# Performance work log

Measured on AMD Instinct MI355X. Metric: run time of the kernel, lower is better.

Reference implementation:

```python
import jax, jax.numpy as jnp
import numpy as np

OUT = 7          # roi_align output size
SR = 2           # sampling_ratio
SCALE = 1.0 / 16.0
T_OUT = 16       # F.interpolate temporal target
EPS = 1e-6


def setup_inputs() -> dict:
    key = jax.random.key(0)
    ks = jax.random.split(key, 12)
    B, Cin, Cout, T, H, W = 1, 1536, 3072, 16, 14, 14
    y = jax.random.normal(ks[0], (B, Cin, T, H, W), jnp.float32)
    x_t = jax.random.normal(ks[1], (B, Cout, T, H, W), jnp.float32)
    # ROIs in 224x224 image coords (spatial_scale = 1/16): one [1,4] box per frame
    x1 = jax.random.uniform(ks[2], (T,), minval=0.0, maxval=112.0)
    y1 = jax.random.uniform(ks[3], (T,), minval=0.0, maxval=112.0)
    x2 = jnp.minimum(x1 + jax.random.uniform(ks[4], (T,), minval=80.0, maxval=112.0), 224.0)
    y2 = jnp.minimum(y1 + jax.random.uniform(ks[5], (T,), minval=80.0, maxval=112.0), 224.0)
    rois = jnp.stack([x1, y1, x2, y2], axis=-1)[:, None, :]  # [T,1,4]
    conv_w = jax.random.normal(ks[6], (Cout, Cin), jnp.float32) * 0.02
    conv_b = jax.random.normal(ks[7], (Cout,), jnp.float32) * 0.02
    gamma = 1.0 + 0.1 * jax.random.normal(ks[8], (Cout,), jnp.float32)
    beta = 0.1 * jax.random.normal(ks[9], (Cout,), jnp.float32)
    run_mean = 0.1 * jax.random.normal(ks[10], (Cout,), jnp.float32)
    run_var = jax.random.uniform(ks[11], (Cout,), minval=0.5, maxval=1.5)
    return dict(y=y, x_t=x_t, rois=rois, conv_w=conv_w, conv_b=conv_b,
                gamma=gamma, beta=beta, run_mean=run_mean, run_var=run_var)


def _bilinear_sample(img, ys, xs):
    # img: [C,H,W]; ys: [Sy]; xs: [Sx] -> [C,Sy,Sx]; torchvision roi_align semantics
    C, H, W = img.shape
    oy = (ys < -1.0) | (ys > H)
    ox = (xs < -1.0) | (xs > W)
    yc = jnp.clip(ys, 0.0, H - 1)
    xc = jnp.clip(xs, 0.0, W - 1)
    y0 = jnp.floor(yc).astype(jnp.int32)
    x0 = jnp.floor(xc).astype(jnp.int32)
    y1i = jnp.minimum(y0 + 1, H - 1)
    x1i = jnp.minimum(x0 + 1, W - 1)
    ly = yc - y0
    lx = xc - x0
    g = lambda yi, xi: img[:, yi[:, None], xi[None, :]]  # [C,Sy,Sx]
    wy0, wy1 = (1.0 - ly)[:, None], ly[:, None]
    wx0, wx1 = (1.0 - lx)[None, :], lx[None, :]
    val = (wy0 * wx0 * g(y0, x0) + wy0 * wx1 * g(y0, x1i)
           + wy1 * wx0 * g(y1i, x0) + wy1 * wx1 * g(y1i, x1i))
    mask = (~oy)[:, None] & (~ox)[None, :]
    return jnp.where(mask[None], val, 0.0)


def _roi_align(feat, boxes):
    # feat: [N,C,H,W]; boxes: [N,4] (one box per image, aligned=False, sampling_ratio=2)
    N, C, H, W = feat.shape
    b = boxes * SCALE
    bx1, by1, bx2, by2 = b[:, 0], b[:, 1], b[:, 2], b[:, 3]
    rw = jnp.maximum(bx2 - bx1, 1.0)
    rh = jnp.maximum(by2 - by1, 1.0)
    bw, bh = rw / OUT, rh / OUT
    # sample positions per bin: (bin + (i+0.5)/SR) * bin_size
    pos = (jnp.arange(OUT, dtype=jnp.float32)[:, None]
           + (jnp.arange(SR, dtype=jnp.float32)[None, :] + 0.5) / SR).reshape(-1)  # [OUT*SR]
    ys = by1[:, None] + pos[None, :] * bh[:, None]
    xs = bx1[:, None] + pos[None, :] * bw[:, None]
    vals = jax.vmap(_bilinear_sample)(feat, ys, xs)  # [N,C,OUT*SR,OUT*SR]
    return vals.reshape(N, C, OUT, SR, OUT, SR).mean(axis=(3, 5))


def reference(y, x_t, rois, conv_w, conv_b, gamma, beta, run_mean, run_var):
    B, Cout, T, Hf, Wf = x_t.shape
    # 1x1x1 Conv3d, stride (1,2,2)
    ys = y[:, :, :, ::2, ::2]                                   # [B,Cin,T,7,7]
    yp = jnp.einsum('bcthw,oc->bothw', ys, conv_w) + conv_b[None, :, None, None, None]
    # BatchNorm3d (eval, eps=1e-6) + GELU (exact)
    inv = gamma / jnp.sqrt(run_var + EPS)
    yp = (yp - run_mean[None, :, None, None, None]) * inv[None, :, None, None, None] \
         + beta[None, :, None, None, None]
    yp = jax.nn.gelu(yp, approximate=False)
    # nearest temporal interpolation to T_OUT (identity when Tin == 16)
    Tin = yp.shape[2]
    tidx = (jnp.arange(T_OUT) * Tin) // T_OUT
    yp = yp[:, :, tidx]                                          # [B,Cout,16,7,7]
    # fusion branch: roi_align over (B*T) frames
    ff = jnp.transpose(x_t, (0, 2, 1, 3, 4)).reshape(B * T, Cout, Hf, Wf)
    boxes = rois[:, 0, :]                                        # [T,4]
    mr = _roi_align(ff, boxes)                                   # [B*T,Cout,7,7]
    mr = jnp.transpose(mr.reshape(B, T, Cout, OUT, OUT), (0, 2, 1, 3, 4))
    weighted = yp * mr                                           # [B,Cout,16,7,7]
    # per-frame 7x7 scatter-write into zeros, same window logic as the torch loop
    bs = boxes * SCALE
    sxi = jnp.floor(bs[:, 0]).astype(jnp.int32)
    syi = jnp.floor(bs[:, 1]).astype(jnp.int32)
    exi = jnp.ceil(bs[:, 2]).astype(jnp.int32)
    eyi = jnp.ceil(bs[:, 3]).astype(jnp.int32)
    ml = jnp.where(sxi + 7 < 14, sxi, exi - 7)
    mt = jnp.where(syi + 7 < 14, syi, eyi - 7)
    def place(w_t, t_off, l_off):  # w_t: [B,Cout,7,7]
        z = jnp.zeros((B, Cout, Hf, Wf), w_t.dtype)
        return jax.lax.dynamic_update_slice(z, w_t, (0, 0, t_off, l_off))
    new_face = jax.vmap(place, in_axes=(2, 0, 0), out_axes=2)(weighted, mt, ml)
    return new_face + x_t
```

## Files before the change

### kernel.cpp

```cpp
#include <hip/hip_runtime.h>

#define KD 1536
#define ND 3072
#define MD 784
#define MPAD 832
#define TT 16

#define NB_ROI 768
#define NB_PACKA 384
#define NB_ZERO 1
#define NB_PACKB 1152
#define PREP_BLOCKS (NB_ROI + NB_PACKA + NB_ZERO + NB_PACKB)

typedef __attribute__((ext_vector_type(8))) short short8;
typedef __attribute__((ext_vector_type(4))) float floatx4;

__device__ __forceinline__ unsigned short f2bf(float f) {
    unsigned int x = __float_as_uint(f);
    unsigned int r = (x + 0x7fffu + ((x >> 16) & 1u)) >> 16;
    return (unsigned short)r;
}

__global__ __launch_bounds__(256) void prep_k(const float* __restrict__ y,
                                              const float* __restrict__ x_t,
                                              const float* __restrict__ rois,
                                              const float* __restrict__ conv_w,
                                              unsigned short* __restrict__ Ap,
                                              unsigned short* __restrict__ Bp,
                                              float* __restrict__ mr) {
    __shared__ float sm[64 * 197];
    __shared__ float wx0s[14], wx1s[14], wy0s[14], wy1s[14];
    __shared__ int x0s[14], x1s[14], y0s[14], y1s[14], vxs[14], vys[14];
    const int bid = blockIdx.x;
    const int tid = threadIdx.x;

    if (bid >= NB_ROI + NB_PACKA + NB_ZERO) {
        int pb = bid - (NB_ROI + NB_PACKA + NB_ZERO);
#pragma unroll
        for (int v = 0; v < 4; ++v) {
            size_t e = (size_t)pb * 4096 + v * 1024 + tid * 4;
            float4 w4 = *(const float4*)(conv_w + e);
            ushort4 o;
            o.x = f2bf(w4.x); o.y = f2bf(w4.y); o.z = f2bf(w4.z); o.w = f2bf(w4.w);
            *(ushort4*)(Bp + e) = o;
        }
        return;
    }
    if (bid == NB_ROI + NB_PACKA) {
        uint4 z = {0u, 0u, 0u, 0u};
        uint4* dst = (uint4*)(Ap + (size_t)MD * KD);
        for (int v = tid; v < (MPAD - MD) * KD / 8; v += 256) dst[v] = z;
        return;
    }
    if (bid >= NB_ROI) {
        int p = bid - NB_ROI;
        int t = p / 24, kc = p % 24;
        for (int f = tid; f < 64 * 196; f += 256) {
            int c = f / 196, pix = f % 196;
            sm[c * 197 + pix] = y[(size_t)(kc * 64 + c) * 3136 + t * 196 + pix];
        }
        __syncthreads();
        for (int item = tid; item < 64 * 49; item += 256) {
            int c = item & 63, ij = item >> 6;
            int i = ij / 7, j = ij % 7;
            Ap[(size_t)(t * 49 + ij) * KD + kc * 64 + c] =
                f2bf(sm[c * 197 + (2 * i) * 14 + 2 * j]);
        }
        return;
    }

    const int t = bid / 48;
    const int o0 = (bid % 48) * 64;

    if (tid < 14) {
        float b0 = rois[t * 4 + 0] * 0.0625f, b1 = rois[t * 4 + 1] * 0.0625f;
        float b2 = rois[t * 4 + 2] * 0.0625f, b3 = rois[t * 4 + 3] * 0.0625f;
        float rw = fmaxf(b2 - b0, 1.0f), rh = fmaxf(b3 - b1, 1.0f);
        float bw = rw * (1.0f / 7.0f), bh = rh * (1.0f / 7.0f);
        int p = tid;
        float pos = (float)(p >> 1) + 0.25f + 0.5f * (float)(p & 1);
        float xs = b0 + pos * bw;
        float ysv = b1 + pos * bh;
        vxs[p] = (xs >= -1.0f && xs <= 14.0f);
        vys[p] = (ysv >= -1.0f && ysv <= 14.0f);
        float xc = fminf(fmaxf(xs, 0.0f), 13.0f);
        float yc = fminf(fmaxf(ysv, 0.0f), 13.0f);
        int x0 = (int)floorf(xc), y0 = (int)floorf(yc);
        x0s[p] = x0; y0s[p] = y0;
        x1s[p] = min(x0 + 1, 13); y1s[p] = min(y0 + 1, 13);
        float lx = xc - (float)x0, ly = yc - (float)y0;
        wx0s[p] = 1.0f - lx; wx1s[p] = lx; wy0s[p] = 1.0f - ly; wy1s[p] = ly;
    }
    for (int f = tid; f < 64 * 196; f += 256) {
        int c = f / 196, pix = f % 196;
        sm[c * 197 + pix] = x_t[(size_t)(o0 + c) * 3136 + t * 196 + pix];
    }
    __syncthreads();
    for (int item = tid; item < 64 * 49; item += 256) {
        int c = item & 63, ij = item >> 6;
        int i = ij / 7, j = ij % 7;
        const float* base = &sm[c * 197];
        float sum = 0.0f;
#pragma unroll
        for (int s = 0; s < 2; ++s) {
            int p = 2 * i + s;
#pragma unroll
            for (int u = 0; u < 2; ++u) {
                int q = 2 * j + u;
                if (vys[p] && vxs[q]) {
                    float v00 = base[y0s[p] * 14 + x0s[q]];
                    float v01 = base[y0s[p] * 14 + x1s[q]];
                    float v10 = base[y1s[p] * 14 + x0s[q]];
                    float v11 = base[y1s[p] * 14 + x1s[q]];
                    sum += wy0s[p] * (wx0s[q] * v00 + wx1s[q] * v01) +
                           wy1s[p] * (wx0s[q] * v10 + wx1s[q] * v11);
                }
            }
        }
        mr[(size_t)(t * 49 + ij) * ND + o0 + c] = 0.25f * sum;
    }
}

__global__ __launch_bounds__(256) void gemm_k(const unsigned short* __restrict__ Ap,
                                              const unsigned short* __restrict__ Bp,
                                              const float* __restrict__ cb,
                                              const float* __restrict__ gm,
                                              const float* __restrict__ bt,
                                              const float* __restrict__ rm,
                                              const float* __restrict__ rv,
                                              float* __restrict__ mrW) {
    __shared__ unsigned short As[2][64][72];
    __shared__ unsigned short Bs[2][64][72];
    const int tid = threadIdx.x;
    const int n0 = blockIdx.x * 64;
    const int m0 = blockIdx.y * 64;
    const int wave = tid >> 6;
    const int lane = tid & 63;
    const int wm = wave >> 1, wn = wave & 1;
    const int l15 = lane & 15, quad = lane >> 4;

    floatx4 acc00 = {0.f, 0.f, 0.f, 0.f}, acc01 = {0.f, 0.f, 0.f, 0.f};
    floatx4 acc10 = {0.f, 0.f, 0.f, 0.f}, acc11 = {0.f, 0.f, 0.f, 0.f};

    const int srow = tid >> 3;
    const int sko = (tid & 7) * 8;
    const float4* agp0 = (const float4*)(Ap + (size_t)(m0 + srow) * KD + sko);
    const float4* agp1 = (const float4*)(Ap + (size_t)(m0 + srow + 32) * KD + sko);
    const float4* bgp0 = (const float4*)(Bp + (size_t)(n0 + srow) * KD + sko);
    const float4* bgp1 = (const float4*)(Bp + (size_t)(n0 + srow + 32) * KD + sko);

    float4 av0 = agp0[0], av1 = agp1[0], bv0 = bgp0[0], bv1 = bgp1[0];

    int p = 0;
    for (int kt = 0; kt < KD; kt += 64, p ^= 1) {
        *(float4*)(&As[p][srow][sko]) = av0;
        *(float4*)(&As[p][srow + 32][sko]) = av1;
        *(float4*)(&Bs[p][srow][sko]) = bv0;
        *(float4*)(&Bs[p][srow + 32][sko]) = bv1;
        __syncthreads();
        if (kt + 64 < KD) {
            int q = (kt >> 3) + 8;
            av0 = agp0[q]; av1 = agp1[q]; bv0 = bgp0[q]; bv1 = bgp1[q];
        }
#pragma unroll
        for (int ko = 0; ko < 2; ++ko) {
            short8 a0 = *(const short8*)(&As[p][wm * 32 + l15][ko * 32 + quad * 8]);
            short8 a1 = *(const short8*)(&As[p][wm * 32 + 16 + l15][ko * 32 + quad * 8]);
            short8 b0 = *(const short8*)(&Bs[p][wn * 32 + l15][ko * 32 + quad * 8]);
            short8 b1 = *(const short8*)(&Bs[p][wn * 32 + 16 + l15][ko * 32 + quad * 8]);
            acc00 = __builtin_amdgcn_mfma_f32_16x16x32_bf16(a0, b0, acc00, 0, 0, 0);
            acc01 = __builtin_amdgcn_mfma_f32_16x16x32_bf16(a0, b1, acc01, 0, 0, 0);
            acc10 = __builtin_amdgcn_mfma_f32_16x16x32_bf16(a1, b0, acc10, 0, 0, 0);
            acc11 = __builtin_amdgcn_mfma_f32_16x16x32_bf16(a1, b1, acc11, 0, 0, 0);
        }
    }

#pragma unroll
    for (int ni = 0; ni < 2; ++ni) {
        int n = n0 + wn * 32 + ni * 16 + l15;
        float scale = gm[n] / sqrtf(rv[n] + 1e-6f);
        float shift = (cb[n] - rm[n]) * scale + bt[n];
#pragma unroll
        for (int mi = 0; mi < 2; ++mi) {
            floatx4 a = (ni == 0) ? (mi == 0 ? acc00 : acc10) : (mi == 0 ? acc01 : acc11);
#pragma unroll
            for (int r = 0; r < 4; ++r) {
                int m = m0 + wm * 32 + mi * 16 + quad * 4 + r;
                if (m < MD) {
                    float v = a[r] * scale + shift;
                    float g = 0.5f * v * (1.0f + erff(v * 0.70710678118654752f));
                    size_t idx = (size_t)m * ND + n;
                    mrW[idx] = g * mrW[idx];
                }
            }
        }
    }
}

__global__ __launch_bounds__(256) void final_k(const float* __restrict__ x_t,
                                               const float* __restrict__ rois,
                                               const float* __restrict__ W,
                                               float* __restrict__ out) {
    __shared__ float Wl[49 * 65];
    const int o0 = blockIdx.x * 64;
    const int t = blockIdx.y;
    const int tid = threadIdx.x;

    float b0 = rois[t * 4 + 0] * 0.0625f, b1 = rois[t * 4 + 1] * 0.0625f;
    float b2 = rois[t * 4 + 2] * 0.0625f, b3 = rois[t * 4 + 3] * 0.0625f;
    int sxi = (int)floorf(b0), syi = (int)floorf(b1);
    int exi = (int)ceilf(b2), eyi = (int)ceilf(b3);
    int ml = (sxi + 7 < 14) ? sxi : exi - 7;
    int mt = (syi + 7 < 14) ? syi : eyi - 7;
    ml = min(max(ml, 0), 7);
    mt = min(max(mt, 0), 7);

    for (int idx = tid; idx < 49 * 64; idx += 256) {
        int c = idx & 63, ij = idx >> 6;
        Wl[ij * 65 + c] = W[(size_t)(t * 49 + ij) * ND + o0 + c];
    }
    __syncthreads();

    for (int i4 = tid; i4 < 3136; i4 += 256) {
        int c = i4 / 49, p4 = i4 % 49;
        size_t e0 = (size_t)(o0 + c) * 3136 + t * 196 + p4 * 4;
        float4 xv = *(const float4*)(x_t + e0);
        float r[4] = {xv.x, xv.y, xv.z, xv.w};
#pragma unroll
        for (int u = 0; u < 4; ++u) {
            int pix = p4 * 4 + u;
            int h = pix / 14, w = pix % 14;
            int i = h - mt, j = w - ml;
            if (i >= 0 && i < 7 && j >= 0 && j < 7)
                r[u] += Wl[(i * 7 + j) * 65 + c];
        }
        *(float4*)(out + e0) = make_float4(r[0], r[1], r[2], r[3]);
    }
}

extern "C" void kernel_launch(void* const* d_in, const int* in_sizes, int n_in,
                              void* d_out, int out_size, void* d_ws, size_t ws_size,
                              hipStream_t stream) {
    const float* y = (const float*)d_in[0];
    const float* x_t = (const float*)d_in[1];
    const float* rois = (const float*)d_in[2];
    const float* conv_w = (const float*)d_in[3];
    const float* conv_b = (const float*)d_in[4];
    const float* gamma = (const float*)d_in[5];
    const float* beta = (const float*)d_in[6];
    const float* run_mean = (const float*)d_in[7];
    const float* run_var = (const float*)d_in[8];
    float* out = (float*)d_out;

    char* ws = (char*)d_ws;
    unsigned short* Ap = (unsigned short*)ws;
    unsigned short* Bp = (unsigned short*)(ws + 2555904);
    float* mrW = (float*)(ws + 2555904 + 9437184);

    prep_k<<<PREP_BLOCKS, 256, 0, stream>>>(y, x_t, rois, conv_w, Ap, Bp, mrW);
    gemm_k<<<dim3(ND / 64, MPAD / 64), 256, 0, stream>>>(Ap, Bp, conv_b, gamma, beta,
                                                         run_mean, run_var, mrW);
    final_k<<<dim3(ND / 64, TT), 256, 0, stream>>>(x_t, rois, mrW, out);
}
```

Measured before the change: 177.8 us.

## Fuse prep, GEMM and scatter into one cooperative kernel with grid sync

Merges the three kernels into one cooperative kernel. Phase A does ROI-align and bf16 packing; after a grid-wide sync, phase B runs a per-frame 64x64 GEMM tile whose GELU-weighted output stays in shared memory and is scatter-added into x_t directly. This removes the intermediate global read-modify-write and the separate final kernel and its launch. In exchange, each GEMM tile computes 64 rows for 49 useful ones and adds a grid barrier. Global loads are also vectorised to float4, and separate kernels serve as a fallback if the cooperative launch fails.

```diff
diff --git a/kernel.cpp b/kernel.cpp
--- a/kernel.cpp
+++ b/kernel.cpp
@@ -1,16 +1,14 @@
 #include <hip/hip_runtime.h>
+#include <hip/hip_cooperative_groups.h>
+
+namespace cg = cooperative_groups;
 
 #define KD 1536
 #define ND 3072
 #define MD 784
 #define MPAD 832
 #define TT 16
-
-#define NB_ROI 768
-#define NB_PACKA 384
-#define NB_ZERO 1
-#define NB_PACKB 1152
-#define PREP_BLOCKS (NB_ROI + NB_PACKA + NB_ZERO + NB_PACKB)
+#define GRID_N 768
 
 typedef __attribute__((ext_vector_type(8))) short short8;
 typedef __attribute__((ext_vector_type(4))) float floatx4;
@@ -21,53 +19,16 @@
     return (unsigned short)r;
 }
 
-__global__ __launch_bounds__(256) void prep_k(const float* __restrict__ y,
-                                              const float* __restrict__ x_t,
-                                              const float* __restrict__ rois,
-                                              const float* __restrict__ conv_w,
-                                              unsigned short* __restrict__ Ap,
-                                              unsigned short* __restrict__ Bp,
-                                              float* __restrict__ mr) {
-    __shared__ float sm[64 * 197];
+__device__ void phaseA(char* smraw,
+                       const float* __restrict__ y, const float* __restrict__ x_t,
+                       const float* __restrict__ rois, const float* __restrict__ conv_w,
+                       unsigned short* __restrict__ Ap, unsigned short* __restrict__ Bp,
+                       float* __restrict__ mr) {
     __shared__ float wx0s[14], wx1s[14], wy0s[14], wy1s[14];
     __shared__ int x0s[14], x1s[14], y0s[14], y1s[14], vxs[14], vys[14];
+    float* sm = (float*)smraw;
     const int bid = blockIdx.x;
     const int tid = threadIdx.x;
-
-    if (bid >= NB_ROI + NB_PACKA + NB_ZERO) {
-        int pb = bid - (NB_ROI + NB_PACKA + NB_ZERO);
-#pragma unroll
-        for (int v = 0; v < 4; ++v) {
-            size_t e = (size_t)pb * 4096 + v * 1024 + tid * 4;
-            float4 w4 = *(const float4*)(conv_w + e);
-            ushort4 o;
-            o.x = f2bf(w4.x); o.y = f2bf(w4.y); o.z = f2bf(w4.z); o.w = f2bf(w4.w);
-            *(ushort4*)(Bp + e) = o;
-        }
-        return;
-    }
-    if (bid == NB_ROI + NB_PACKA) {
-        uint4 z = {0u, 0u, 0u, 0u};
-        uint4* dst = (uint4*)(Ap + (size_t)MD * KD);
-        for (int v = tid; v < (MPAD - MD) * KD / 8; v += 256) dst[v] = z;
-        return;
-    }
-    if (bid >= NB_ROI) {
-        int p = bid - NB_ROI;
-        int t = p / 24, kc = p % 24;
-        for (int f = tid; f < 64 * 196; f += 256) {
-            int c = f / 196, pix = f % 196;
-            sm[c * 197 + pix] = y[(size_t)(kc * 64 + c) * 3136 + t * 196 + pix];
-        }
-        __syncthreads();
-        for (int item = tid; item < 64 * 49; item += 256) {
-            int c = item & 63, ij = item >> 6;
-            int i = ij / 7, j = ij % 7;
-            Ap[(size_t)(t * 49 + ij) * KD + kc * 64 + c] =
-                f2bf(sm[c * 197 + (2 * i) * 14 + 2 * j]);
-        }
-        return;
-    }
 
     const int t = bid / 48;
     const int o0 = (bid % 48) * 64;
@@ -91,9 +52,11 @@
         float lx = xc - (float)x0, ly = yc - (float)y0;
         wx0s[p] = 1.0f - lx; wx1s[p] = lx; wy0s[p] = 1.0f - ly; wy1s[p] = ly;
     }
-    for (int f = tid; f < 64 * 196; f += 256) {
-        int c = f / 196, pix = f % 196;
-        sm[c * 197 + pix] = x_t[(size_t)(o0 + c) * 3136 + t * 196 + pix];
+    for (int f4 = tid; f4 < 64 * 49; f4 += 256) {
+        int c = f4 / 49, p = f4 % 49;
+        float4 v = *(const float4*)(x_t + (size_t)(o0 + c) * 3136 + t * 196 + p * 4);
+        float* d = sm + c * 197 + p * 4;
+        d[0] = v.x; d[1] = v.y; d[2] = v.z; d[3] = v.w;
     }
     __syncthreads();
     for (int item = tid; item < 64 * 49; item += 256) {
@@ -119,21 +82,56 @@
         }
         mr[(size_t)(t * 49 + ij) * ND + o0 + c] = 0.25f * sum;
     }
-}
-
-__global__ __launch_bounds__(256) void gemm_k(const unsigned short* __restrict__ Ap,
-                                              const unsigned short* __restrict__ Bp,
-                                              const float* __restrict__ cb,
-                                              const float* __restrict__ gm,
-                                              const float* __restrict__ bt,
-                                              const float* __restrict__ rm,
-                                              const float* __restrict__ rv,
-                                              float* __restrict__ mrW) {
-    __shared__ unsigned short As[2][64][72];
-    __shared__ unsigned short Bs[2][64][72];
+
+    if (bid < 384) {
+        __syncthreads();
+        int t2 = bid / 24, kc = bid % 24;
+        for (int f4 = tid; f4 < 64 * 49; f4 += 256) {
+            int c = f4 / 49, p = f4 % 49;
+            float4 v = *(const float4*)(y + (size_t)(kc * 64 + c) * 3136 + t2 * 196 + p * 4);
+            float* d = sm + c * 197 + p * 4;
+            d[0] = v.x; d[1] = v.y; d[2] = v.z; d[3] = v.w;
+        }
+        __syncthreads();
+        for (int item = tid; item < 64 * 49; item += 256) {
+            int c = item & 63, ij = item >> 6;
+            int i = ij / 7, j = ij % 7;
+            Ap[(size_t)(t2 * 49 + ij) * KD + kc * 64 + c] =
+                f2bf(sm[c * 197 + (2 * i) * 14 + 2 * j]);
+        }
+    } else {
+        size_t base = (size_t)(bid - 384) * 12288;
+#pragma unroll
+        for (int v = 0; v < 12; ++v) {
+            size_t e = base + v * 1024 + tid * 4;
+            float4 w4 = *(const float4*)(conv_w + e);
+            ushort4 o;
+            o.x = f2bf(w4.x); o.y = f2bf(w4.y); o.z = f2bf(w4.z); o.w = f2bf(w4.w);
+            *(ushort4*)(Bp + e) = o;
+        }
+        if (tid < 24) {
+            uint4 z = {0u, 0u, 0u, 0u};
+            ((uint4*)(Ap + (size_t)MD * KD))[(size_t)(bid - 384) * 24 + tid] = z;
+        }
+    }
+}
+
+__device__ void phaseB(char* smraw,
+                       const unsigned short* __restrict__ Ap,
+                       const unsigned short* __restrict__ Bp,
+                       const float* __restrict__ mr,
+                       const float* __restrict__ x_t, const float* __restrict__ rois,
+                       const float* __restrict__ cb, const float* __restrict__ gm,
+                       const float* __restrict__ bt, const float* __restrict__ rm,
+                       const float* __restrict__ rv,
+                       float* __restrict__ out) {
+    unsigned short* As0 = (unsigned short*)smraw;
+    unsigned short* Bs0 = (unsigned short*)(smraw + 18432);
+    const int bid = blockIdx.x;
     const int tid = threadIdx.x;
-    const int n0 = blockIdx.x * 64;
-    const int m0 = blockIdx.y * 64;
+    const int t = bid / 48;
+    const int n0 = (bid % 48) * 64;
+    const int m0g = t * 49;
     const int wave = tid >> 6;
     const int lane = tid & 63;
     const int wm = wave >> 1, wn = wave & 1;
@@ -144,8 +142,8 @@
 
     const int srow = tid >> 3;
     const int sko = (tid & 7) * 8;
-    const float4* agp0 = (const float4*)(Ap + (size_t)(m0 + srow) * KD + sko);
-    const float4* agp1 = (const float4*)(Ap + (size_t)(m0 + srow + 32) * KD + sko);
+    const float4* agp0 = (const float4*)(Ap + (size_t)(m0g + srow) * KD + sko);
+    const float4* agp1 = (const float4*)(Ap + (size_t)(m0g + srow + 32) * KD + sko);
     const float4* bgp0 = (const float4*)(Bp + (size_t)(n0 + srow) * KD + sko);
     const float4* bgp1 = (const float4*)(Bp + (size_t)(n0 + srow + 32) * KD + sko);
 
@@ -153,10 +151,10 @@
 
     int p = 0;
     for (int kt = 0; kt < KD; kt += 64, p ^= 1) {
-        *(float4*)(&As[p][srow][sko]) = av0;
-        *(float4*)(&As[p][srow + 32][sko]) = av1;
-        *(float4*)(&Bs[p][srow][sko]) = bv0;
-        *(float4*)(&Bs[p][srow + 32][sko]) = bv1;
+        *(float4*)(&As0[p * 4608 + srow * 72 + sko]) = av0;
+        *(float4*)(&As0[p * 4608 + (srow + 32) * 72 + sko]) = av1;
+        *(float4*)(&Bs0[p * 4608 + srow * 72 + sko]) = bv0;
+        *(float4*)(&Bs0[p * 4608 + (srow + 32) * 72 + sko]) = bv1;
         __syncthreads();
         if (kt + 64 < KD) {
             int q = (kt >> 3) + 8;
@@ -164,20 +162,23 @@
         }
 #pragma unroll
         for (int ko = 0; ko < 2; ++ko) {
-            short8 a0 = *(const short8*)(&As[p][wm * 32 + l15][ko * 32 + quad * 8]);
-            short8 a1 = *(const short8*)(&As[p][wm * 32 + 16 + l15][ko * 32 + quad * 8]);
-            short8 b0 = *(const short8*)(&Bs[p][wn * 32 + l15][ko * 32 + quad * 8]);
-            short8 b1 = *(const short8*)(&Bs[p][wn * 32 + 16 + l15][ko * 32 + quad * 8]);
+            short8 a0 = *(const short8*)(&As0[p * 4608 + (wm * 32 + l15) * 72 + ko * 32 + quad * 8]);
+            short8 a1 = *(const short8*)(&As0[p * 4608 + (wm * 32 + 16 + l15) * 72 + ko * 32 + quad * 8]);
+            short8 b0 = *(const short8*)(&Bs0[p * 4608 + (wn * 32 + l15) * 72 + ko * 32 + quad * 8]);
+            short8 b1 = *(const short8*)(&Bs0[p * 4608 + (wn * 32 + 16 + l15) * 72 + ko * 32 + quad * 8]);
             acc00 = __builtin_amdgcn_mfma_f32_16x16x32_bf16(a0, b0, acc00, 0, 0, 0);
             acc01 = __builtin_amdgcn_mfma_f32_16x16x32_bf16(a0, b1, acc01, 0, 0, 0);
             acc10 = __builtin_amdgcn_mfma_f32_16x16x32_bf16(a1, b0, acc10, 0, 0, 0);
             acc11 = __builtin_amdgcn_mfma_f32_16x16x32_bf16(a1, b1, acc11, 0, 0, 0);
         }
     }
-
+    __syncthreads();
+
+    float* Wl = (float*)smraw;
 #pragma unroll
     for (int ni = 0; ni < 2; ++ni) {
-        int n = n0 + wn * 32 + ni * 16 + l15;
+        int nl = wn * 32 + ni * 16 + l15;
+        int n = n0 + nl;
         float scale = gm[n] / sqrtf(rv[n] + 1e-6f);
         float shift = (cb[n] - rm[n]) * scale + bt[n];
 #pragma unroll
@@ -185,26 +186,16 @@
             floatx4 a = (ni == 0) ? (mi == 0 ? acc00 : acc10) : (mi == 0 ? acc01 : acc11);
 #pragma unroll
             for (int r = 0; r < 4; ++r) {
-                int m = m0 + wm * 32 + mi * 16 + quad * 4 + r;
-                if (m < MD) {
+                int ml_ = wm * 32 + mi * 16 + quad * 4 + r;
+                if (ml_ < 49) {
                     float v = a[r] * scale + shift;
                     float g = 0.5f * v * (1.0f + erff(v * 0.70710678118654752f));
-                    size_t idx = (size_t)m * ND + n;
-                    mrW[idx] = g * mrW[idx];
+                    Wl[ml_ * 65 + nl] = g * mr[(size_t)(m0g + ml_) * ND + n];
                 }
             }
         }
     }
-}
-
-__global__ __launch_bounds__(256) void final_k(const float* __restrict__ x_t,
-                                               const float* __restrict__ rois,
-                                               const float* __restrict__ W,
-                                               float* __restrict__ out) {
-    __shared__ float Wl[49 * 65];
-    const int o0 = blockIdx.x * 64;
-    const int t = blockIdx.y;
-    const int tid = threadIdx.x;
+    __syncthreads();
 
     float b0 = rois[t * 4 + 0] * 0.0625f, b1 = rois[t * 4 + 1] * 0.0625f;
     float b2 = rois[t * 4 + 2] * 0.0625f, b3 = rois[t * 4 + 3] * 0.0625f;
@@ -215,15 +206,9 @@
     ml = min(max(ml, 0), 7);
     mt = min(max(mt, 0), 7);
 
-    for (int idx = tid; idx < 49 * 64; idx += 256) {
-        int c = idx & 63, ij = idx >> 6;
-        Wl[ij * 65 + c] = W[(size_t)(t * 49 + ij) * ND + o0 + c];
-    }
-    __syncthreads();
-
-    for (int i4 = tid; i4 < 3136; i4 += 256) {
+    for (int i4 = tid; i4 < 64 * 49; i4 += 256) {
         int c = i4 / 49, p4 = i4 % 49;
-        size_t e0 = (size_t)(o0 + c) * 3136 + t * 196 + p4 * 4;
+        size_t e0 = (size_t)(n0 + c) * 3136 + t * 196 + p4 * 4;
         float4 xv = *(const float4*)(x_t + e0);
         float r[4] = {xv.x, xv.y, xv.z, xv.w};
 #pragma unroll
@@ -236,6 +221,39 @@
         }
         *(float4*)(out + e0) = make_float4(r[0], r[1], r[2], r[3]);
     }
+}
+
+__global__ __launch_bounds__(256, 3) void fused_k(const float* y, const float* x_t,
+                                                  const float* rois, const float* conv_w,
+                                                  const float* cb, const float* gm,
+                                                  const float* bt, const float* rm,
+                                                  const float* rv,
+                                                  unsigned short* Ap, unsigned short* Bp,
+                                                  float* mr, float* out) {
+    __shared__ alignas(16) char smraw[50432];
+    phaseA(smraw, y, x_t, rois, conv_w, Ap, Bp, mr);
+    __threadfence();
+    cg::this_grid().sync();
+    phaseB(smraw, Ap, Bp, mr, x_t, rois, cb, gm, bt, rm, rv, out);
+}
+
+__global__ __launch_bounds__(256, 3) void prepA_k(const float* y, const float* x_t,
+                                                  const float* rois, const float* conv_w,
+                                                  unsigned short* Ap, unsigned short* Bp,
+                                                  float* mr) {
+    __shared__ alignas(16) char smraw[50432];
+    phaseA(smraw, y, x_t, rois, conv_w, Ap, Bp, mr);
+}
+
+__global__ __launch_bounds__(256, 3) void gemmB_k(const unsigned short* Ap,
+                                                  const unsigned short* Bp,
+                                                  const float* mr, const float* x_t,
+                                                  const float* rois, const float* cb,
+                                                  const float* gm, const float* bt,
+                                                  const float* rm, const float* rv,
+                                                  float* out) {
+    __shared__ alignas(16) char smraw[50432];
+    phaseB(smraw, Ap, Bp, mr, x_t, rois, cb, gm, bt, rm, rv, out);
 }
 
 extern "C" void kernel_launch(void* const* d_in, const int* in_sizes, int n_in,
@@ -245,20 +263,25 @@
     const float* x_t = (const float*)d_in[1];
     const float* rois = (const float*)d_in[2];
     const float* conv_w = (const float*)d_in[3];
-    const float* conv_b = (const float*)d_in[4];
-    const float* gamma = (const float*)d_in[5];
-    const float* beta = (const float*)d_in[6];
-    const float* run_mean = (const float*)d_in[7];
-    const float* run_var = (const float*)d_in[8];
+    const float* cb = (const float*)d_in[4];
+    const float* gm = (const float*)d_in[5];
+    const float* bt = (const float*)d_in[6];
+    const float* rm = (const float*)d_in[7];
+    const float* rv = (const float*)d_in[8];
     float* out = (float*)d_out;
 
     char* ws = (char*)d_ws;
     unsigned short* Ap = (unsigned short*)ws;
     unsigned short* Bp = (unsigned short*)(ws + 2555904);
-    float* mrW = (float*)(ws + 2555904 + 9437184);
-
-    prep_k<<<PREP_BLOCKS, 256, 0, stream>>>(y, x_t, rois, conv_w, Ap, Bp, mrW);
-    gemm_k<<<dim3(ND / 64, MPAD / 64), 256, 0, stream>>>(Ap, Bp, conv_b, gamma, beta,
-                                                         run_mean, run_var, mrW);
-    final_k<<<dim3(ND / 64, TT), 256, 0, stream>>>(x_t, rois, mrW, out);
-}
+    float* mr = (float*)(ws + 2555904 + 9437184);
+
+    void* args[] = {(void*)&y, (void*)&x_t, (void*)&rois, (void*)&conv_w,
+                    (void*)&cb, (void*)&gm, (void*)&bt, (void*)&rm, (void*)&rv,
+                    (void*)&Ap, (void*)&Bp, (void*)&mr, (void*)&out};
+    hipError_t err = hipLaunchCooperativeKernel((const void*)fused_k, dim3(GRID_N),
+                                                dim3(256), args, 0, stream);
+    if (err != hipSuccess) {
+        prepA_k<<<GRID_N, 256, 0, stream>>>(y, x_t, rois, conv_w, Ap, Bp, mr);
+        gemmB_k<<<GRID_N, 256, 0, stream>>>(Ap, Bp, mr, x_t, rois, cb, gm, bt, rm, rv, out);
+    }
+}
```

After: 400.8 us. 2.25x slower.

## Load GEMM tiles directly into swizzled LDS and merge prep work per block

Applied to the files above, without the earlier changes.

The GEMM now stages A and B tiles with global_load_lds, copying straight from global memory into LDS with no register round trip. The LDS layout drops the padded rows and uses an XOR swizzle to avoid bank conflicts, and launch bounds ask for 4 blocks per CU. The prep kernel now runs 768 blocks that each do ROI-align work and then either the activation packing or a larger slice of the weight conversion, replacing the separate specialised blocks. The block that zeroed the GEMM padding rows is removed, so rows past 784 now read whatever is left in the workspace; this relies on those output rows being discarded.

```diff
diff --git a/kernel.cpp b/kernel.cpp
--- a/kernel.cpp
+++ b/kernel.cpp
@@ -3,14 +3,7 @@
 #define KD 1536
 #define ND 3072
 #define MD 784
-#define MPAD 832
 #define TT 16
-
-#define NB_ROI 768
-#define NB_PACKA 384
-#define NB_ZERO 1
-#define NB_PACKB 1152
-#define PREP_BLOCKS (NB_ROI + NB_PACKA + NB_ZERO + NB_PACKB)
 
 typedef __attribute__((ext_vector_type(8))) short short8;
 typedef __attribute__((ext_vector_type(4))) float floatx4;
@@ -19,6 +12,11 @@
     unsigned int x = __float_as_uint(f);
     unsigned int r = (x + 0x7fffu + ((x >> 16) & 1u)) >> 16;
     return (unsigned short)r;
+}
+
+__device__ __forceinline__ void gld_lds16(const unsigned short* g, unsigned short* l) {
+    __builtin_amdgcn_global_load_lds((const __attribute__((address_space(1))) void*)g,
+                                     (__attribute__((address_space(3))) void*)l, 16, 0, 0);
 }
 
 __global__ __launch_bounds__(256) void prep_k(const float* __restrict__ y,
@@ -33,41 +31,6 @@
     __shared__ int x0s[14], x1s[14], y0s[14], y1s[14], vxs[14], vys[14];
     const int bid = blockIdx.x;
     const int tid = threadIdx.x;
-
-    if (bid >= NB_ROI + NB_PACKA + NB_ZERO) {
-        int pb = bid - (NB_ROI + NB_PACKA + NB_ZERO);
-#pragma unroll
-        for (int v = 0; v < 4; ++v) {
-            size_t e = (size_t)pb * 4096 + v * 1024 + tid * 4;
-            float4 w4 = *(const float4*)(conv_w + e);
-            ushort4 o;
-            o.x = f2bf(w4.x); o.y = f2bf(w4.y); o.z = f2bf(w4.z); o.w = f2bf(w4.w);
-            *(ushort4*)(Bp + e) = o;
-        }
-        return;
-    }
-    if (bid == NB_ROI + NB_PACKA) {
-        uint4 z = {0u, 0u, 0u, 0u};
-        uint4* dst = (uint4*)(Ap + (size_t)MD * KD);
-        for (int v = tid; v < (MPAD - MD) * KD / 8; v += 256) dst[v] = z;
-        return;
-    }
-    if (bid >= NB_ROI) {
-        int p = bid - NB_ROI;
-        int t = p / 24, kc = p % 24;
-        for (int f = tid; f < 64 * 196; f += 256) {
-            int c = f / 196, pix = f % 196;
-            sm[c * 197 + pix] = y[(size_t)(kc * 64 + c) * 3136 + t * 196 + pix];
-        }
-        __syncthreads();
-        for (int item = tid; item < 64 * 49; item += 256) {
-            int c = item & 63, ij = item >> 6;
-            int i = ij / 7, j = ij % 7;
-            Ap[(size_t)(t * 49 + ij) * KD + kc * 64 + c] =
-                f2bf(sm[c * 197 + (2 * i) * 14 + 2 * j]);
-        }
-        return;
-    }
 
     const int t = bid / 48;
     const int o0 = (bid % 48) * 64;
@@ -119,55 +82,92 @@
         }
         mr[(size_t)(t * 49 + ij) * ND + o0 + c] = 0.25f * sum;
     }
-}
-
-__global__ __launch_bounds__(256) void gemm_k(const unsigned short* __restrict__ Ap,
-                                              const unsigned short* __restrict__ Bp,
-                                              const float* __restrict__ cb,
-                                              const float* __restrict__ gm,
-                                              const float* __restrict__ bt,
-                                              const float* __restrict__ rm,
-                                              const float* __restrict__ rv,
-                                              float* __restrict__ mrW) {
-    __shared__ unsigned short As[2][64][72];
-    __shared__ unsigned short Bs[2][64][72];
+
+    if (bid < 384) {
+        __syncthreads();
+        int t2 = bid / 24, kc = bid % 24;
+        for (int f = tid; f < 64 * 196; f += 256) {
+            int c = f / 196, pix = f % 196;
+            sm[c * 197 + pix] = y[(size_t)(kc * 64 + c) * 3136 + t2 * 196 + pix];
+        }
+        __syncthreads();
+        for (int item = tid; item < 64 * 49; item += 256) {
+            int c = item & 63, ij = item >> 6;
+            int i = ij / 7, j = ij % 7;
+            Ap[(size_t)(t2 * 49 + ij) * KD + kc * 64 + c] =
+                f2bf(sm[c * 197 + (2 * i) * 14 + 2 * j]);
+        }
+    } else {
+        size_t base = (size_t)(bid - 384) * 12288;
+#pragma unroll
+        for (int v = 0; v < 12; ++v) {
+            size_t e = base + v * 1024 + tid * 4;
+            float4 w4 = *(const float4*)(conv_w + e);
+            ushort4 o;
+            o.x = f2bf(w4.x); o.y = f2bf(w4.y); o.z = f2bf(w4.z); o.w = f2bf(w4.w);
+            *(ushort4*)(Bp + e) = o;
+        }
+    }
+}
+
+__global__ __launch_bounds__(256, 4) void gemm_k(const unsigned short* __restrict__ Ap,
+                                                 const unsigned short* __restrict__ Bp,
+                                                 const float* __restrict__ cb,
+                                                 const float* __restrict__ gm,
+                                                 const float* __restrict__ bt,
+                                                 const float* __restrict__ rm,
+                                                 const float* __restrict__ rv,
+                                                 float* __restrict__ mrW) {
+    __shared__ unsigned short As[2][64 * 64];
+    __shared__ unsigned short Bs[2][64 * 64];
     const int tid = threadIdx.x;
     const int n0 = blockIdx.x * 64;
     const int m0 = blockIdx.y * 64;
-    const int wave = tid >> 6;
+    const int wv = tid >> 6;
     const int lane = tid & 63;
-    const int wm = wave >> 1, wn = wave & 1;
+    const int wm = wv >> 1, wn = wv & 1;
     const int l15 = lane & 15, quad = lane >> 4;
+    const int prow = lane >> 3, pch = lane & 7;
+    const int L = pch ^ (prow & 7);
+
+    const unsigned short* gbase;
+    unsigned short *lb0, *lb1;
+    if (wv < 2) {
+        gbase = Ap + (size_t)(m0 + wv * 32 + prow) * KD + L * 8;
+        lb0 = &As[0][(wv * 32) * 64];
+        lb1 = &As[1][(wv * 32) * 64];
+    } else {
+        gbase = Bp + (size_t)(n0 + (wv - 2) * 32 + prow) * KD + L * 8;
+        lb0 = &Bs[0][((wv - 2) * 32) * 64];
+        lb1 = &Bs[1][((wv - 2) * 32) * 64];
+    }
 
     floatx4 acc00 = {0.f, 0.f, 0.f, 0.f}, acc01 = {0.f, 0.f, 0.f, 0.f};
     floatx4 acc10 = {0.f, 0.f, 0.f, 0.f}, acc11 = {0.f, 0.f, 0.f, 0.f};
 
-    const int srow = tid >> 3;
-    const int sko = (tid & 7) * 8;
-    const float4* agp0 = (const float4*)(Ap + (size_t)(m0 + srow) * KD + sko);
-    const float4* agp1 = (const float4*)(Ap + (size_t)(m0 + srow + 32) * KD + sko);
-    const float4* bgp0 = (const float4*)(Bp + (size_t)(n0 + srow) * KD + sko);
-    const float4* bgp1 = (const float4*)(Bp + (size_t)(n0 + srow + 32) * KD + sko);
-
-    float4 av0 = agp0[0], av1 = agp1[0], bv0 = bgp0[0], bv1 = bgp1[0];
+#pragma unroll
+    for (int j = 0; j < 4; ++j)
+        gld_lds16(gbase + (size_t)j * 8 * KD, lb0 + j * 512);
 
     int p = 0;
     for (int kt = 0; kt < KD; kt += 64, p ^= 1) {
-        *(float4*)(&As[p][srow][sko]) = av0;
-        *(float4*)(&As[p][srow + 32][sko]) = av1;
-        *(float4*)(&Bs[p][srow][sko]) = bv0;
-        *(float4*)(&Bs[p][srow + 32][sko]) = bv1;
         __syncthreads();
         if (kt + 64 < KD) {
-            int q = (kt >> 3) + 8;
-            av0 = agp0[q]; av1 = agp1[q]; bv0 = bgp0[q]; bv1 = bgp1[q];
-        }
+            unsigned short* lb = p ? lb0 : lb1;
+            const unsigned short* gb = gbase + kt + 64;
+#pragma unroll
+            for (int j = 0; j < 4; ++j)
+                gld_lds16(gb + (size_t)j * 8 * KD, lb + j * 512);
+        }
+        const unsigned short* Ab = &As[p][0];
+        const unsigned short* Bb = &Bs[p][0];
 #pragma unroll
         for (int ko = 0; ko < 2; ++ko) {
-            short8 a0 = *(const short8*)(&As[p][wm * 32 + l15][ko * 32 + quad * 8]);
-            short8 a1 = *(const short8*)(&As[p][wm * 32 + 16 + l15][ko * 32 + quad * 8]);
-            short8 b0 = *(const short8*)(&Bs[p][wn * 32 + l15][ko * 32 + quad * 8]);
-            short8 b1 = *(const short8*)(&Bs[p][wn * 32 + 16 + l15][ko * 32 + quad * 8]);
+            int ch = ((ko * 4 + quad) ^ (l15 & 7)) * 8;
+            short8 a0 = *(const short8*)(Ab + (wm * 32 + l15) * 64 + ch);
+            short8 a1 = *(const short8*)(Ab + (wm * 32 + 16 + l15) * 64 + ch);
+            short8 b0 = *(const short8*)(Bb + (wn * 32 + l15) * 64 + ch);
+            short8 b1 = *(const short8*)(Bb + (wn * 32 + 16 + l15) * 64 + ch);
             acc00 = __builtin_amdgcn_mfma_f32_16x16x32_bf16(a0, b0, acc00, 0, 0, 0);
             acc01 = __builtin_amdgcn_mfma_f32_16x16x32_bf16(a0, b1, acc01, 0, 0, 0);
             acc10 = __builtin_amdgcn_mfma_f32_16x16x32_bf16(a1, b0, acc10, 0, 0, 0);
@@ -245,11 +245,11 @@
     const float* x_t = (const float*)d_in[1];
     const float* rois = (const float*)d_in[2];
     const float* conv_w = (const float*)d_in[3];
-    const float* conv_b = (const float*)d_in[4];
-    const float* gamma = (const float*)d_in[5];
-    const float* beta = (const float*)d_in[6];
-    const float* run_mean = (const float*)d_in[7];
-    const float* run_var = (const float*)d_in[8];
+    const float* cb = (const float*)d_in[4];
+    const float* gm = (const float*)d_in[5];
+    const float* bt = (const float*)d_in[6];
+    const float* rm = (const float*)d_in[7];
+    const float* rv = (const float*)d_in[8];
     float* out = (float*)d_out;
 
     char* ws = (char*)d_ws;
@@ -257,8 +257,7 @@
     unsigned short* Bp = (unsigned short*)(ws + 2555904);
     float* mrW = (float*)(ws + 2555904 + 9437184);
 
-    prep_k<<<PREP_BLOCKS, 256, 0, stream>>>(y, x_t, rois, conv_w, Ap, Bp, mrW);
-    gemm_k<<<dim3(ND / 64, MPAD / 64), 256, 0, stream>>>(Ap, Bp, conv_b, gamma, beta,
-                                                         run_mean, run_var, mrW);
+    prep_k<<<768, 256, 0, stream>>>(y, x_t, rois, conv_w, Ap, Bp, mrW);
+    gemm_k<<<dim3(ND / 64, 13), 256, 0, stream>>>(Ap, Bp, cb, gm, bt, rm, rv, mrW);
     final_k<<<dim3(ND / 64, TT), 256, 0, stream>>>(x_t, rois, mrW, out);
 }
```

Measured after the change: 175.6 us. About the same (-1.2%).
